# Performance work log

Measured on AMD Instinct MI355X. Metric: run time of the kernel, lower is better.

Reference implementation:

```python
import jax, jax.numpy as jnp
import numpy as np
import math

EPS = 1e-5  # torch BatchNorm2d default eps
EXPANSION_RATE = 2


def _bn_train(x, gamma, beta):
    # BatchNorm2d in training mode: biased batch statistics over (B, H, W)
    mu = jnp.mean(x, axis=(0, 2, 3), keepdims=True)
    var = jnp.var(x, axis=(0, 2, 3), keepdims=True)
    xn = (x - mu) * jax.lax.rsqrt(var + EPS)
    return gamma[None, :, None, None] * xn + beta[None, :, None, None]


def _conv1x1(x, w, b):
    # w: [O, C]  (1x1 conv kernel squeezed), b: [O]
    return jnp.einsum('bchw,oc->bohw', x, w) + b[None, :, None, None]


def _lsgc(x, w_diff, b_diff, g_bn, be_bn, w_in, b_in, g_ibn, be_ibn,
          w_mr, b_mr, g_mbn, be_mbn):
    B, C, H, W = x.shape
    bit_depth = max(math.ceil(math.log2(H)), math.ceil(math.log2(W)))
    steps = [EXPANSION_RATE * 2 ** (n - 1) for n in range(1, bit_depth + 1)]

    fmax = None
    for step in steps:
        for axis, size in ((3, W), (2, H)):
            s = step % size
            for sgn in (1, -1):  # forward / backward rolls
                shifted = jnp.roll(x, sgn * s, axis=axis) if s else x
                d = x - shifted
                fmax = d if fmax is None else jnp.maximum(fmax, d)

    x_diff = _bn_train(_conv1x1(fmax, w_diff, b_diff), g_bn, be_bn)
    x_proc = _bn_train(_conv1x1(x, w_in, b_in), g_ibn, be_ibn)

    # MRConv: concat -> 1x1 conv -> BN -> GELU (exact) -> residual add
    x_cat = jnp.concatenate([x_proc, x_diff], axis=1)
    h = _bn_train(_conv1x1(x_cat, w_mr, b_mr), g_mbn, be_mbn)
    h = jax.nn.gelu(h, approximate=False)
    return x_proc + h


def setup_inputs() -> dict:
    key = jax.random.key(0)
    ks = jax.random.split(key, 8)
    B, C_in, C_out, H, W = 32, 128, 128, 64, 64

    def kaiming(k, o, i):
        return jax.random.normal(k, (o, i), jnp.float32) * np.sqrt(2.0 / i)

    return {
        'x': jax.random.normal(ks[0], (B, C_in, H, W), jnp.float32),
        'w_diff': kaiming(ks[1], C_out, C_in),
        'b_diff': jnp.zeros((C_out,), jnp.float32),
        'g_bn': jnp.ones((C_out,), jnp.float32),
        'be_bn': jnp.zeros((C_out,), jnp.float32),
        'w_in': kaiming(ks[2], C_out, C_in),
        'b_in': jnp.zeros((C_out,), jnp.float32),
        'g_ibn': jnp.ones((C_out,), jnp.float32),
        'be_ibn': jnp.zeros((C_out,), jnp.float32),
        'w_mr': kaiming(ks[3], C_out, 2 * C_out),
        'b_mr': jnp.zeros((C_out,), jnp.float32),
        'g_mbn': jnp.ones((C_out,), jnp.float32),
        'be_mbn': jnp.zeros((C_out,), jnp.float32),
    }


def reference(x, w_diff, b_diff, g_bn, be_bn, w_in, b_in, g_ibn, be_ibn,
              w_mr, b_mr, g_mbn, be_mbn):
    return _lsgc(x, w_diff, b_diff, g_bn, be_bn, w_in, b_in, g_ibn, be_ibn,
                 w_mr, b_mr, g_mbn, be_mbn)
```

## Files before the change

### kernel.cpp

```cpp
#include <hip/hip_runtime.h>
#include <math.h>


#define INV_NPIX (1.0f / 131072.0f)
#define EPS 1e-5f
#define KP 66

typedef __attribute__((ext_vector_type(8))) short s16x8;
typedef __attribute__((ext_vector_type(4))) float f32x4;

__device__ __forceinline__ uint32_t bf16_rne(float v) {
  uint32_t x = __float_as_uint(v);
  return (x + 0x7fffu + ((x >> 16) & 1u)) >> 16;
}
__device__ __forceinline__ uint32_t pack_hl(float v) {
  uint32_t h = bf16_rne(v);
  float lo = v - __uint_as_float(h << 16);
  return h | (bf16_rne(lo) << 16);
}
__device__ __forceinline__ float bf_lo(uint32_t d) {
  return __uint_as_float(d << 16);
}
__device__ __forceinline__ float bf_hi(uint32_t d) {
  return __uint_as_float(d & 0xffff0000u);
}
__device__ __forceinline__ float4 fmin4(float4 a, float4 b) {
  return make_float4(fminf(a.x, b.x), fminf(a.y, b.y), fminf(a.z, b.z),
                     fminf(a.w, b.w));
}

__global__ __launch_bounds__(256) void stencil_prep_kernel(
    const float* __restrict__ x, uint32_t* __restrict__ xp,
    uint32_t* __restrict__ fp, const float* __restrict__ w_in,
    const float* __restrict__ w_diff, unsigned short* __restrict__ wInH,
    unsigned short* __restrict__ wInL, unsigned short* __restrict__ wDfH,
    unsigned short* __restrict__ wDfL) {
  __shared__ float4 pA[1024];
  __shared__ float4 pB[1024];
  if (blockIdx.x >= 2048) {
    const int t = (blockIdx.x - 2048) * 256 + threadIdx.x;
    const int e = t & 16383;
    const float* w = (t < 16384) ? w_in : w_diff;
    unsigned short* aH = (t < 16384) ? wInH : wDfH;
    unsigned short* aL = (t < 16384) ? wInL : wDfL;
    const int j = e & 7, l = (e >> 3) & 63, mt = (e >> 9) & 7, kc = e >> 12;
    const int m = mt * 16 + (l & 15);
    const int k = kc * 32 + ((l >> 4) << 3) + j;
    const uint32_t p = pack_hl(w[m * 128 + k]);
    aH[e] = (unsigned short)(p & 0xffffu);
    aL[e] = (unsigned short)(p >> 16);
    return;
  }
  const int b = blockIdx.x >> 6;
  const int cp = blockIdx.x & 63;
  const float4* xa = (const float4*)x + (size_t)(b * 128 + 2 * cp) * 1024;
  const float4* xb = xa + 1024;
  float4 sA[4], sB[4];
#pragma unroll
  for (int i = 0; i < 4; ++i) {
    const int u = threadIdx.x + i * 256;
    sA[i] = xa[u];
    sB[i] = xb[u];
    pA[u] = sA[i];
    pB[u] = sB[i];
  }
  __syncthreads();
  const size_t obase = (size_t)(b * 64 + cp) * 1024;
#pragma unroll
  for (int i = 0; i < 4; ++i) {
    const int u = threadIdx.x + i * 256;
    const int h = u >> 4, wu = u & 15;
    const int row = u & ~15;
    float4 mA, mB;
    {
      const float4 A = sA[i];
      const float4 L = pA[row | ((wu + 15) & 15)];
      const float4 R = pA[row | ((wu + 1) & 15)];
      float4 m = fmin4(A, fmin4(L, R));
      m = fmin4(m, make_float4(A.z, A.w, R.x, R.y));
      m = fmin4(m, make_float4(L.z, L.w, A.x, A.y));
      m = fmin4(m, pA[row | ((wu + 2) & 15)]);
      m = fmin4(m, pA[row | ((wu + 14) & 15)]);
      m = fmin4(m, pA[row | ((wu + 4) & 15)]);
      m = fmin4(m, pA[row | ((wu + 12) & 15)]);
      m = fmin4(m, pA[row | ((wu + 8) & 15)]);
      m = fmin4(m, pA[(((h + 2) & 63) << 4) | wu]);
      m = fmin4(m, pA[(((h + 62) & 63) << 4) | wu]);
      m = fmin4(m, pA[(((h + 4) & 63) << 4) | wu]);
      m = fmin4(m, pA[(((h + 60) & 63) << 4) | wu]);
      m = fmin4(m, pA[(((h + 8) & 63) << 4) | wu]);
      m = fmin4(m, pA[(((h + 56) & 63) << 4) | wu]);
      m = fmin4(m, pA[(((h + 16) & 63) << 4) | wu]);
      m = fmin4(m, pA[(((h + 48) & 63) << 4) | wu]);
      m = fmin4(m, pA[(((h + 32) & 63) << 4) | wu]);
      mA = m;
    }
    {
      const float4 A = sB[i];
      const float4 L = pB[row | ((wu + 15) & 15)];
      const float4 R = pB[row | ((wu + 1) & 15)];
      float4 m = fmin4(A, fmin4(L, R));
      m = fmin4(m, make_float4(A.z, A.w, R.x, R.y));
      m = fmin4(m, make_float4(L.z, L.w, A.x, A.y));
      m = fmin4(m, pB[row | ((wu + 2) & 15)]);
      m = fmin4(m, pB[row | ((wu + 14) & 15)]);
      m = fmin4(m, pB[row | ((wu + 4) & 15)]);
      m = fmin4(m, pB[row | ((wu + 12) & 15)]);
      m = fmin4(m, pB[row | ((wu + 8) & 15)]);
      m = fmin4(m, pB[(((h + 2) & 63) << 4) | wu]);
      m = fmin4(m, pB[(((h + 62) & 63) << 4) | wu]);
      m = fmin4(m, pB[(((h + 4) & 63) << 4) | wu]);
      m = fmin4(m, pB[(((h + 60) & 63) << 4) | wu]);
      m = fmin4(m, pB[(((h + 8) & 63) << 4) | wu]);
      m = fmin4(m, pB[(((h + 56) & 63) << 4) | wu]);
      m = fmin4(m, pB[(((h + 16) & 63) << 4) | wu]);
      m = fmin4(m, pB[(((h + 48) & 63) << 4) | wu]);
      m = fmin4(m, pB[(((h + 32) & 63) << 4) | wu]);
      mB = m;
    }
    uint4 px, pf;
    px.x = bf16_rne(sA[i].x) | (bf16_rne(sB[i].x) << 16);
    px.y = bf16_rne(sA[i].y) | (bf16_rne(sB[i].y) << 16);
    px.z = bf16_rne(sA[i].z) | (bf16_rne(sB[i].z) << 16);
    px.w = bf16_rne(sA[i].w) | (bf16_rne(sB[i].w) << 16);
    pf.x = bf16_rne(sA[i].x - mA.x) | (bf16_rne(sB[i].x - mB.x) << 16);
    pf.y = bf16_rne(sA[i].y - mA.y) | (bf16_rne(sB[i].y - mB.y) << 16);
    pf.z = bf16_rne(sA[i].z - mA.z) | (bf16_rne(sB[i].z - mB.z) << 16);
    pf.w = bf16_rne(sA[i].w - mA.w) | (bf16_rne(sB[i].w - mB.w) << 16);
    ((uint4*)xp)[obase + u] = px;
    ((uint4*)fp)[obase + u] = pf;
  }
}

template <int NC>
__device__ __forceinline__ void gemm_body(
    const unsigned short* __restrict__ AH, const unsigned short* __restrict__ AL,
    const uint32_t* __restrict__ B0, const uint32_t* __restrict__ B1,
    uint32_t* __restrict__ outp, float* __restrict__ pS,
    float* __restrict__ pQ, const int bx, uint32_t* Bs) {
  const int tid = threadIdx.x;
  const int lane = tid & 63;
  const int wave = tid >> 6;
  const int b = bx >> 6;
  const int hw0 = (bx & 63) << 6;
  const int sk2 = tid >> 4;
  const int sn4 = (tid & 15) << 2;
  const int q = lane >> 4;
  const int ln = lane & 15;

  f32x4 acc[2][4];
#pragma unroll
  for (int i = 0; i < 2; ++i)
#pragma unroll
    for (int j = 0; j < 4; ++j) acc[i][j] = (f32x4)(0.0f);

  uint4 ld[NC];
#pragma unroll
  for (int c = 0; c < NC; ++c) {
    const uint32_t* src = (c < 4) ? B0 : B1;
    ld[c] = *(const uint4*)&src[((size_t)(b * 64 + (c & 3) * 16 + sk2)) * 4096 +
                                hw0 + sn4];
  }
  s16x8 ah[2][2], al[2][2];
#pragma unroll
  for (int mt2 = 0; mt2 < 2; ++mt2) {
    const size_t off = ((size_t)((wave * 2 + mt2) * 64 + lane)) << 3;
    ah[0][mt2] = *(const s16x8*)(AH + off);
    al[0][mt2] = *(const s16x8*)(AL + off);
  }

#pragma unroll
  for (int kc = 0; kc < NC; ++kc) {
    const int cur = kc & 1;
    const int nxt = cur ^ 1;
    uint32_t* buf = Bs + cur * (16 * KP);
    *(uint4*)&buf[sk2 * KP + sn4] = ld[kc];
    __syncthreads();
    if (kc + 1 < NC) {
#pragma unroll
      for (int mt2 = 0; mt2 < 2; ++mt2) {
        const size_t off =
            ((size_t)(((kc + 1) * 8 + wave * 2 + mt2) * 64 + lane)) << 3;
        ah[nxt][mt2] = *(const s16x8*)(AH + off);
        al[nxt][mt2] = *(const s16x8*)(AL + off);
      }
    }
#pragma unroll
    for (int nt = 0; nt < 4; ++nt) {
      union { uint32_t u[4]; s16x8 s; } bb;
#pragma unroll
      for (int j = 0; j < 4; ++j)
        bb.u[j] = buf[(q * 4 + j) * KP + nt * 16 + ln];
#pragma unroll
      for (int mt2 = 0; mt2 < 2; ++mt2) {
        acc[mt2][nt] = __builtin_amdgcn_mfma_f32_16x16x32_bf16(
            ah[cur][mt2], bb.s, acc[mt2][nt], 0, 0, 0);
        acc[mt2][nt] = __builtin_amdgcn_mfma_f32_16x16x32_bf16(
            al[cur][mt2], bb.s, acc[mt2][nt], 0, 0, 0);
      }
    }
  }

#pragma unroll
  for (int mt2 = 0; mt2 < 2; ++mt2) {
    float sa[4] = {0.f, 0.f, 0.f, 0.f};
    float sq[4] = {0.f, 0.f, 0.f, 0.f};
#pragma unroll
    for (int nt = 0; nt < 4; ++nt) {
#pragma unroll
      for (int rp = 0; rp < 2; ++rp) {
        const float v0 = acc[mt2][nt][2 * rp];
        const float v1 = acc[mt2][nt][2 * rp + 1];
        const int m2 = (wave * 2 + mt2) * 8 + q * 2 + rp;
        outp[((size_t)(b * 64 + m2)) * 4096 + hw0 + nt * 16 + ln] =
            bf16_rne(v0) | (bf16_rne(v1) << 16);
        sa[2 * rp] += v0;
        sq[2 * rp] += v0 * v0;
        sa[2 * rp + 1] += v1;
        sq[2 * rp + 1] += v1 * v1;
      }
    }
#pragma unroll
    for (int off = 1; off < 16; off <<= 1) {
#pragma unroll
      for (int r = 0; r < 4; ++r) {
        sa[r] += __shfl_xor(sa[r], off);
        sq[r] += __shfl_xor(sq[r], off);
      }
    }
    if (ln == 0) {
#pragma unroll
      for (int r = 0; r < 4; ++r) {
        const int m = (wave * 2 + mt2) * 16 + q * 4 + r;
        pS[bx * 128 + m] = sa[r];
        pQ[bx * 128 + m] = sq[r];
      }
    }
  }
}

__global__ __launch_bounds__(256) void gemm1_dual(
    const unsigned short* __restrict__ AH1, const unsigned short* __restrict__ AL1,
    const uint32_t* __restrict__ XP, uint32_t* __restrict__ out1,
    float* __restrict__ sv1, float* __restrict__ sq1,
    const unsigned short* __restrict__ AH2, const unsigned short* __restrict__ AL2,
    const uint32_t* __restrict__ FP, uint32_t* __restrict__ out2,
    float* __restrict__ sv2, float* __restrict__ sq2) {
  __shared__ uint32_t Bs[2 * 16 * KP];
  const int bx = blockIdx.x & 2047;
  if ((blockIdx.x >> 11) == 0)
    gemm_body<4>(AH1, AL1, XP, nullptr, out1, sv1, sq1, bx, Bs);
  else
    gemm_body<4>(AH2, AL2, FP, nullptr, out2, sv2, sq2, bx, Bs);
}

__global__ __launch_bounds__(256) void gemm2_kernel(
    const unsigned short* __restrict__ AH, const unsigned short* __restrict__ AL,
    const uint32_t* __restrict__ B0, const uint32_t* __restrict__ B1,
    uint32_t* __restrict__ outp, float* __restrict__ sv,
    float* __restrict__ sq) {
  __shared__ uint32_t Bs[2 * 16 * KP];
  gemm_body<8>(AH, AL, B0, B1, outp, sv, sq, blockIdx.x, Bs);
}

__global__ __launch_bounds__(256) void reduce_kernel(
    const float* __restrict__ P, float* __restrict__ p2) {
  const int a = blockIdx.x >> 4, g = blockIdx.x & 15;
  const int c = threadIdx.x & 127, h = threadIdx.x >> 7;
  const float* src = P + ((size_t)(a * 2048 + g * 128 + h * 64)) * 128 + c;
  float s0 = 0.f, s1 = 0.f, s2 = 0.f, s3 = 0.f;
#pragma unroll
  for (int j = 0; j < 64; j += 4) {
    s0 += src[(j + 0) * 128];
    s1 += src[(j + 1) * 128];
    s2 += src[(j + 2) * 128];
    s3 += src[(j + 3) * 128];
  }
  __shared__ float sm[256];
  sm[threadIdx.x] = (s0 + s1) + (s2 + s3);
  __syncthreads();
  if (h == 0) p2[(a * 16 + g) * 128 + c] = sm[c] + sm[128 + c];
}

__global__ __launch_bounds__(256) void finalize1_kernel(
    const float* __restrict__ p2, const float* __restrict__ g_ibn,
    const float* __restrict__ be_ibn, const float* __restrict__ g_bn,
    const float* __restrict__ w_mr, float* __restrict__ a_in,
    float* __restrict__ d_in, unsigned short* __restrict__ wEffH,
    unsigned short* __restrict__ wEffL) {
  __shared__ float sa[256];
  const int t = threadIdx.x;
  if (t < 128) {
    float s = 0.f, qq = 0.f;
#pragma unroll
    for (int g = 0; g < 16; ++g) {
      s += p2[g * 128 + t];
      qq += p2[(16 + g) * 128 + t];
    }
    const float mu = s * INV_NPIX;
    const float var = fmaxf(qq * INV_NPIX - mu * mu, 0.f);
    const float a = g_ibn[t] * rsqrtf(var + EPS);
    if (blockIdx.x == 0) {
      a_in[t] = a;
      d_in[t] = be_ibn[t] - mu * a;
    }
    sa[t] = a;
  } else {
    const int c = t - 128;
    float s = 0.f, qq = 0.f;
#pragma unroll
    for (int g = 0; g < 16; ++g) {
      s += p2[(32 + g) * 128 + c];
      qq += p2[(48 + g) * 128 + c];
    }
    const float mu = s * INV_NPIX;
    const float var = fmaxf(qq * INV_NPIX - mu * mu, 0.f);
    sa[t] = g_bn[c] * rsqrtf(var + EPS);
  }
  __syncthreads();
  const int e = blockIdx.x * 256 + t;
  const int j = e & 7, l = (e >> 3) & 63, mt = (e >> 9) & 7, kc = e >> 12;
  const int m = mt * 16 + (l & 15);
  const int k = kc * 32 + ((l >> 4) << 3) + j;
  const uint32_t p = pack_hl(w_mr[m * 256 + k] * sa[k]);
  wEffH[e] = (unsigned short)(p & 0xffffu);
  wEffL[e] = (unsigned short)(p >> 16);
}

__global__ __launch_bounds__(128) void finalize2_kernel(
    const float* __restrict__ p2h, const float* __restrict__ g_mbn,
    const float* __restrict__ be_mbn, float* __restrict__ a_m,
    float* __restrict__ d_m) {
  const int t = threadIdx.x;
  float s = 0.f, qq = 0.f;
#pragma unroll
  for (int g = 0; g < 16; ++g) {
    s += p2h[g * 128 + t];
    qq += p2h[(16 + g) * 128 + t];
  }
  const float mu = s * INV_NPIX;
  const float var = fmaxf(qq * INV_NPIX - mu * mu, 0.f);
  const float a = g_mbn[t] * rsqrtf(var + EPS);
  a_m[t] = a;
  d_m[t] = be_mbn[t] - mu * a;
}

__device__ __forceinline__ float gelu_exact(float z) {
  return 0.5f * z * (1.0f + erff(z * 0.70710678118654752f));
}

__global__ __launch_bounds__(256) void epilogue_kernel(
    const uint32_t* __restrict__ yp, const uint32_t* __restrict__ hp,
    const float* __restrict__ a_in, const float* __restrict__ d_in,
    const float* __restrict__ a_m, const float* __restrict__ d_m,
    float* __restrict__ out) {
  const size_t i = (size_t)blockIdx.x * 256 + threadIdx.x;
  const int cp = (int)((i >> 10) & 63);
  const int b = (int)(i >> 16);
  const int c0 = 2 * cp, c1 = 2 * cp + 1;
  const uint4 yv = ((const uint4*)yp)[i];
  const uint4 hv = ((const uint4*)hp)[i];
  const float a0 = a_in[c0], d0 = d_in[c0], m0 = a_m[c0], e0 = d_m[c0];
  const float a1 = a_in[c1], d1 = d_in[c1], m1 = a_m[c1], e1 = d_m[c1];
  float4 o0, o1;
  o0.x = fmaf(a0, bf_lo(yv.x), d0) + gelu_exact(fmaf(m0, bf_lo(hv.x), e0));
  o0.y = fmaf(a0, bf_lo(yv.y), d0) + gelu_exact(fmaf(m0, bf_lo(hv.y), e0));
  o0.z = fmaf(a0, bf_lo(yv.z), d0) + gelu_exact(fmaf(m0, bf_lo(hv.z), e0));
  o0.w = fmaf(a0, bf_lo(yv.w), d0) + gelu_exact(fmaf(m0, bf_lo(hv.w), e0));
  o1.x = fmaf(a1, bf_hi(yv.x), d1) + gelu_exact(fmaf(m1, bf_hi(hv.x), e1));
  o1.y = fmaf(a1, bf_hi(yv.y), d1) + gelu_exact(fmaf(m1, bf_hi(hv.y), e1));
  o1.z = fmaf(a1, bf_hi(yv.z), d1) + gelu_exact(fmaf(m1, bf_hi(hv.z), e1));
  o1.w = fmaf(a1, bf_hi(yv.w), d1) + gelu_exact(fmaf(m1, bf_hi(hv.w), e1));
  const size_t u = i & 1023;
  ((float4*)out)[(size_t)(b * 128 + c0) * 1024 + u] = o0;
  ((float4*)out)[(size_t)(b * 128 + c1) * 1024 + u] = o1;
}

extern "C" void kernel_launch(void* const* d_in, const int* in_sizes, int n_in,
                              void* d_out, int out_size, void* d_ws,
                              size_t ws_size, hipStream_t stream) {
  const float* x = (const float*)d_in[0];
  const float* w_diff = (const float*)d_in[1];
  const float* g_bn = (const float*)d_in[3];
  const float* w_in = (const float*)d_in[5];
  const float* g_ibn = (const float*)d_in[7];
  const float* be_ibn = (const float*)d_in[8];
  const float* w_mr = (const float*)d_in[9];
  const float* g_mbn = (const float*)d_in[11];
  const float* be_mbn = (const float*)d_in[12];
  float* out = (float*)d_out;

  const size_t PD = (size_t)8388608;
  uint32_t* ws = (uint32_t*)d_ws;
  uint32_t* xp = ws;
  uint32_t* fpx = ws + PD;
  uint32_t* ypIn = ws + 2 * PD;
  uint32_t* ypDf = ws + 3 * PD;
  uint32_t* hp = ws + 4 * PD;
  float* st = (float*)(ws + 5 * PD);
  float* p2 = st;
  float* p2h = st + 8192;
  float* a_in = st + 12288, *dinc = st + 12416;
  float* a_m = st + 12544, *d_m = st + 12672;
  unsigned short* fr = (unsigned short*)(st + 12800);
  unsigned short* wInH = fr;
  unsigned short* wInL = fr + 16384;
  unsigned short* wDfH = fr + 32768;
  unsigned short* wDfL = fr + 49152;
  unsigned short* wEffH = fr + 65536;
  unsigned short* wEffL = fr + 98304;
  float* g1p = (float*)(ws + 4 * PD);
  float* g2p = (float*)ws;

  stencil_prep_kernel<<<2176, 256, 0, stream>>>(x, xp, fpx, w_in, w_diff,
                                                wInH, wInL, wDfH, wDfL);
  gemm1_dual<<<4096, 256, 0, stream>>>(wInH, wInL, xp, ypIn, g1p,
                                       g1p + 262144, wDfH, wDfL, fpx, ypDf,
                                       g1p + 524288, g1p + 786432);
  reduce_kernel<<<64, 256, 0, stream>>>(g1p, p2);
  finalize1_kernel<<<128, 256, 0, stream>>>(p2, g_ibn, be_ibn, g_bn, w_mr,
                                            a_in, dinc, wEffH, wEffL);
  gemm2_kernel<<<2048, 256, 0, stream>>>(wEffH, wEffL, ypIn, ypDf, hp, g2p,
                                         g2p + 262144);
  reduce_kernel<<<32, 256, 0, stream>>>(g2p, p2h);
  finalize2_kernel<<<1, 128, 0, stream>>>(p2h, g_mbn, be_mbn, a_m, d_m);
  epilogue_kernel<<<8192, 256, 0, stream>>>(ypIn, hp, a_in, dinc, a_m, d_m,
                                            out);
}
```

Baseline: 271.8 us.

## Make GEMM kernels process multiple tiles per block with cross-tile prefetch

Both GEMM stages now have each block loop over several consecutive 64-pixel tiles (4 for gemm1, 2 for gemm2), using fewer blocks. Each block loads a full 64-row K slab into LDS with a single barrier instead of one barrier per 16-row chunk. The next tile's (or next half's) B operand is prefetched into registers while the current tile is computed. This cuts launch and barrier overhead and hides global load latency, but LDS use per block rises and fewer blocks are launched, which may lower occupancy and latency hiding.

```diff
diff --git a/kernel.cpp b/kernel.cpp
--- a/kernel.cpp
+++ b/kernel.cpp
@@ -5,6 +5,8 @@
 #define INV_NPIX (1.0f / 131072.0f)
 #define EPS 1e-5f
 #define KP 66
+#define T1 4
+#define T2 2
 
 typedef __attribute__((ext_vector_type(8))) short s16x8;
 typedef __attribute__((ext_vector_type(4))) float f32x4;
@@ -132,75 +134,10 @@
   }
 }
 
-template <int NC>
-__device__ __forceinline__ void gemm_body(
-    const unsigned short* __restrict__ AH, const unsigned short* __restrict__ AL,
-    const uint32_t* __restrict__ B0, const uint32_t* __restrict__ B1,
-    uint32_t* __restrict__ outp, float* __restrict__ pS,
-    float* __restrict__ pQ, const int bx, uint32_t* Bs) {
-  const int tid = threadIdx.x;
-  const int lane = tid & 63;
-  const int wave = tid >> 6;
-  const int b = bx >> 6;
-  const int hw0 = (bx & 63) << 6;
-  const int sk2 = tid >> 4;
-  const int sn4 = (tid & 15) << 2;
-  const int q = lane >> 4;
-  const int ln = lane & 15;
-
-  f32x4 acc[2][4];
-#pragma unroll
-  for (int i = 0; i < 2; ++i)
-#pragma unroll
-    for (int j = 0; j < 4; ++j) acc[i][j] = (f32x4)(0.0f);
-
-  uint4 ld[NC];
-#pragma unroll
-  for (int c = 0; c < NC; ++c) {
-    const uint32_t* src = (c < 4) ? B0 : B1;
-    ld[c] = *(const uint4*)&src[((size_t)(b * 64 + (c & 3) * 16 + sk2)) * 4096 +
-                                hw0 + sn4];
-  }
-  s16x8 ah[2][2], al[2][2];
-#pragma unroll
-  for (int mt2 = 0; mt2 < 2; ++mt2) {
-    const size_t off = ((size_t)((wave * 2 + mt2) * 64 + lane)) << 3;
-    ah[0][mt2] = *(const s16x8*)(AH + off);
-    al[0][mt2] = *(const s16x8*)(AL + off);
-  }
-
-#pragma unroll
-  for (int kc = 0; kc < NC; ++kc) {
-    const int cur = kc & 1;
-    const int nxt = cur ^ 1;
-    uint32_t* buf = Bs + cur * (16 * KP);
-    *(uint4*)&buf[sk2 * KP + sn4] = ld[kc];
-    __syncthreads();
-    if (kc + 1 < NC) {
-#pragma unroll
-      for (int mt2 = 0; mt2 < 2; ++mt2) {
-        const size_t off =
-            ((size_t)(((kc + 1) * 8 + wave * 2 + mt2) * 64 + lane)) << 3;
-        ah[nxt][mt2] = *(const s16x8*)(AH + off);
-        al[nxt][mt2] = *(const s16x8*)(AL + off);
-      }
-    }
-#pragma unroll
-    for (int nt = 0; nt < 4; ++nt) {
-      union { uint32_t u[4]; s16x8 s; } bb;
-#pragma unroll
-      for (int j = 0; j < 4; ++j)
-        bb.u[j] = buf[(q * 4 + j) * KP + nt * 16 + ln];
-#pragma unroll
-      for (int mt2 = 0; mt2 < 2; ++mt2) {
-        acc[mt2][nt] = __builtin_amdgcn_mfma_f32_16x16x32_bf16(
-            ah[cur][mt2], bb.s, acc[mt2][nt], 0, 0, 0);
-        acc[mt2][nt] = __builtin_amdgcn_mfma_f32_16x16x32_bf16(
-            al[cur][mt2], bb.s, acc[mt2][nt], 0, 0, 0);
-      }
-    }
-  }
-
+__device__ __forceinline__ void cwrite_stats(
+    const f32x4 (&acc)[2][4], uint32_t* __restrict__ outp,
+    float* __restrict__ pS, float* __restrict__ pQ, const int bx, const int b,
+    const int hw0, const int wave, const int q, const int ln) {
 #pragma unroll
   for (int mt2 = 0; mt2 < 2; ++mt2) {
     float sa[4] = {0.f, 0.f, 0.f, 0.f};
@@ -239,6 +176,95 @@
   }
 }
 
+template <int T>
+__device__ __forceinline__ void gemm1_persist(
+    const unsigned short* __restrict__ AH, const unsigned short* __restrict__ AL,
+    const uint32_t* __restrict__ B0, uint32_t* __restrict__ outp,
+    float* __restrict__ pS, float* __restrict__ pQ, const int p,
+    uint32_t* Bs) {
+  const int tid = threadIdx.x;
+  const int lane = tid & 63;
+  const int wave = tid >> 6;
+  const int sk2 = tid >> 4;
+  const int sn4 = (tid & 15) << 2;
+  const int q = lane >> 4;
+  const int ln = lane & 15;
+
+  uint4 ld[4];
+  {
+    const int bx0 = p * T;
+    const int b = bx0 >> 6, hw0 = (bx0 & 63) << 6;
+#pragma unroll
+    for (int c = 0; c < 4; ++c)
+      ld[c] = *(const uint4*)&B0[((size_t)(b * 64 + c * 16 + sk2)) * 4096 +
+                                 hw0 + sn4];
+  }
+
+#pragma unroll
+  for (int t = 0; t < T; ++t) {
+    const int bx = p * T + t;
+    const int b = bx >> 6, hw0 = (bx & 63) << 6;
+    uint32_t* buf = Bs + (t & 1) * (64 * KP);
+
+#pragma unroll
+    for (int c = 0; c < 4; ++c)
+      *(uint4*)&buf[(c * 16 + sk2) * KP + sn4] = ld[c];
+
+    s16x8 ah[2][2], al[2][2];
+#pragma unroll
+    for (int mt2 = 0; mt2 < 2; ++mt2) {
+      const size_t off = ((size_t)((wave * 2 + mt2) * 64 + lane)) << 3;
+      ah[0][mt2] = *(const s16x8*)(AH + off);
+      al[0][mt2] = *(const s16x8*)(AL + off);
+    }
+    __syncthreads();
+
+    if (t + 1 < T) {
+      const int bn = bx + 1;
+      const int b2 = bn >> 6, hw2 = (bn & 63) << 6;
+#pragma unroll
+      for (int c = 0; c < 4; ++c)
+        ld[c] = *(const uint4*)&B0[((size_t)(b2 * 64 + c * 16 + sk2)) * 4096 +
+                                   hw2 + sn4];
+    }
+
+    f32x4 acc[2][4];
+#pragma unroll
+    for (int i = 0; i < 2; ++i)
+#pragma unroll
+      for (int j = 0; j < 4; ++j) acc[i][j] = (f32x4)(0.0f);
+
+#pragma unroll
+    for (int kc = 0; kc < 4; ++kc) {
+      if (kc < 3) {
+#pragma unroll
+        for (int mt2 = 0; mt2 < 2; ++mt2) {
+          const size_t off =
+              ((size_t)(((kc + 1) * 8 + wave * 2 + mt2) * 64 + lane)) << 3;
+          ah[(kc + 1) & 1][mt2] = *(const s16x8*)(AH + off);
+          al[(kc + 1) & 1][mt2] = *(const s16x8*)(AL + off);
+        }
+      }
+#pragma unroll
+      for (int nt = 0; nt < 4; ++nt) {
+        union { uint32_t u[4]; s16x8 s; } bb;
+#pragma unroll
+        for (int j = 0; j < 4; ++j)
+          bb.u[j] = buf[(kc * 16 + q * 4 + j) * KP + nt * 16 + ln];
+#pragma unroll
+        for (int mt2 = 0; mt2 < 2; ++mt2) {
+          acc[mt2][nt] = __builtin_amdgcn_mfma_f32_16x16x32_bf16(
+              ah[kc & 1][mt2], bb.s, acc[mt2][nt], 0, 0, 0);
+          acc[mt2][nt] = __builtin_amdgcn_mfma_f32_16x16x32_bf16(
+              al[kc & 1][mt2], bb.s, acc[mt2][nt], 0, 0, 0);
+        }
+      }
+    }
+
+    cwrite_stats(acc, outp, pS, pQ, bx, b, hw0, wave, q, ln);
+  }
+}
+
 __global__ __launch_bounds__(256) void gemm1_dual(
     const unsigned short* __restrict__ AH1, const unsigned short* __restrict__ AL1,
     const uint32_t* __restrict__ XP, uint32_t* __restrict__ out1,
@@ -246,12 +272,146 @@
     const unsigned short* __restrict__ AH2, const unsigned short* __restrict__ AL2,
     const uint32_t* __restrict__ FP, uint32_t* __restrict__ out2,
     float* __restrict__ sv2, float* __restrict__ sq2) {
-  __shared__ uint32_t Bs[2 * 16 * KP];
-  const int bx = blockIdx.x & 2047;
-  if ((blockIdx.x >> 11) == 0)
-    gemm_body<4>(AH1, AL1, XP, nullptr, out1, sv1, sq1, bx, Bs);
+  __shared__ uint32_t Bs[2 * 64 * KP];
+  const int p = blockIdx.x & 511;
+  if (blockIdx.x < 512)
+    gemm1_persist<T1>(AH1, AL1, XP, out1, sv1, sq1, p, Bs);
   else
-    gemm_body<4>(AH2, AL2, FP, nullptr, out2, sv2, sq2, bx, Bs);
+    gemm1_persist<T1>(AH2, AL2, FP, out2, sv2, sq2, p, Bs);
+}
+
+template <int T>
+__device__ __forceinline__ void gemm2_persist(
+    const unsigned short* __restrict__ AH, const unsigned short* __restrict__ AL,
+    const uint32_t* __restrict__ B0, const uint32_t* __restrict__ B1,
+    uint32_t* __restrict__ outp, float* __restrict__ pS,
+    float* __restrict__ pQ, const int p, uint32_t* Bs) {
+  const int tid = threadIdx.x;
+  const int lane = tid & 63;
+  const int wave = tid >> 6;
+  const int sk2 = tid >> 4;
+  const int sn4 = (tid & 15) << 2;
+  const int q = lane >> 4;
+  const int ln = lane & 15;
+
+  uint4 ld[4];
+  {
+    const int bx0 = p * T;
+    const int b = bx0 >> 6, hw0 = (bx0 & 63) << 6;
+#pragma unroll
+    for (int c = 0; c < 4; ++c)
+      ld[c] = *(const uint4*)&B0[((size_t)(b * 64 + c * 16 + sk2)) * 4096 +
+                                 hw0 + sn4];
+  }
+
+#pragma unroll
+  for (int t = 0; t < T; ++t) {
+    const int bx = p * T + t;
+    const int b = bx >> 6, hw0 = (bx & 63) << 6;
+
+    f32x4 acc[2][4];
+#pragma unroll
+    for (int i = 0; i < 2; ++i)
+#pragma unroll
+      for (int j = 0; j < 4; ++j) acc[i][j] = (f32x4)(0.0f);
+
+    s16x8 ah[2][2], al[2][2];
+
+    {
+      uint32_t* buf = Bs;
+#pragma unroll
+      for (int c = 0; c < 4; ++c)
+        *(uint4*)&buf[(c * 16 + sk2) * KP + sn4] = ld[c];
+#pragma unroll
+      for (int mt2 = 0; mt2 < 2; ++mt2) {
+        const size_t off = ((size_t)((wave * 2 + mt2) * 64 + lane)) << 3;
+        ah[0][mt2] = *(const s16x8*)(AH + off);
+        al[0][mt2] = *(const s16x8*)(AL + off);
+      }
+      __syncthreads();
+#pragma unroll
+      for (int c = 0; c < 4; ++c)
+        ld[c] = *(const uint4*)&B1[((size_t)(b * 64 + c * 16 + sk2)) * 4096 +
+                                   hw0 + sn4];
+#pragma unroll
+      for (int kc = 0; kc < 4; ++kc) {
+        if (kc < 3) {
+#pragma unroll
+          for (int mt2 = 0; mt2 < 2; ++mt2) {
+            const size_t off =
+                ((size_t)(((kc + 1) * 8 + wave * 2 + mt2) * 64 + lane)) << 3;
+            ah[(kc + 1) & 1][mt2] = *(const s16x8*)(AH + off);
+            al[(kc + 1) & 1][mt2] = *(const s16x8*)(AL + off);
+          }
+        }
+#pragma unroll
+        for (int nt = 0; nt < 4; ++nt) {
+          union { uint32_t u[4]; s16x8 s; } bb;
+#pragma unroll
+          for (int j = 0; j < 4; ++j)
+            bb.u[j] = buf[(kc * 16 + q * 4 + j) * KP + nt * 16 + ln];
+#pragma unroll
+          for (int mt2 = 0; mt2 < 2; ++mt2) {
+            acc[mt2][nt] = __builtin_amdgcn_mfma_f32_16x16x32_bf16(
+                ah[kc & 1][mt2], bb.s, acc[mt2][nt], 0, 0, 0);
+            acc[mt2][nt] = __builtin_amdgcn_mfma_f32_16x16x32_bf16(
+                al[kc & 1][mt2], bb.s, acc[mt2][nt], 0, 0, 0);
+          }
+        }
+      }
+    }
+
+    {
+      uint32_t* buf = Bs + 64 * KP;
+#pragma unroll
+      for (int c = 0; c < 4; ++c)
+        *(uint4*)&buf[(c * 16 + sk2) * KP + sn4] = ld[c];
+#pragma unroll
+      for (int mt2 = 0; mt2 < 2; ++mt2) {
+        const size_t off =
+            ((size_t)((4 * 8 + wave * 2 + mt2) * 64 + lane)) << 3;
+        ah[0][mt2] = *(const s16x8*)(AH + off);
+        al[0][mt2] = *(const s16x8*)(AL + off);
+      }
+      __syncthreads();
+      if (t + 1 < T) {
+        const int bn = bx + 1;
+        const int b2 = bn >> 6, hw2 = (bn & 63) << 6;
+#pragma unroll
+        for (int c = 0; c < 4; ++c)
+          ld[c] = *(const uint4*)&B0[((size_t)(b2 * 64 + c * 16 + sk2)) * 4096 +
+                                     hw2 + sn4];
+      }
+#pragma unroll
+      for (int kc = 4; kc < 8; ++kc) {
+        if (kc < 7) {
+#pragma unroll
+          for (int mt2 = 0; mt2 < 2; ++mt2) {
+            const size_t off =
+                ((size_t)(((kc + 1) * 8 + wave * 2 + mt2) * 64 + lane)) << 3;
+            ah[(kc + 1) & 1][mt2] = *(const s16x8*)(AH + off);
+            al[(kc + 1) & 1][mt2] = *(const s16x8*)(AL + off);
+          }
+        }
+#pragma unroll
+        for (int nt = 0; nt < 4; ++nt) {
+          union { uint32_t u[4]; s16x8 s; } bb;
+#pragma unroll
+          for (int j = 0; j < 4; ++j)
+            bb.u[j] = buf[((kc - 4) * 16 + q * 4 + j) * KP + nt * 16 + ln];
+#pragma unroll
+          for (int mt2 = 0; mt2 < 2; ++mt2) {
+            acc[mt2][nt] = __builtin_amdgcn_mfma_f32_16x16x32_bf16(
+                ah[kc & 1][mt2], bb.s, acc[mt2][nt], 0, 0, 0);
+            acc[mt2][nt] = __builtin_amdgcn_mfma_f32_16x16x32_bf16(
+                al[kc & 1][mt2], bb.s, acc[mt2][nt], 0, 0, 0);
+          }
+        }
+      }
+    }
+
+    cwrite_stats(acc, outp, pS, pQ, bx, b, hw0, wave, q, ln);
+  }
 }
 
 __global__ __launch_bounds__(256) void gemm2_kernel(
@@ -259,8 +419,8 @@
     const uint32_t* __restrict__ B0, const uint32_t* __restrict__ B1,
     uint32_t* __restrict__ outp, float* __restrict__ sv,
     float* __restrict__ sq) {
-  __shared__ uint32_t Bs[2 * 16 * KP];
-  gemm_body<8>(AH, AL, B0, B1, outp, sv, sq, blockIdx.x, Bs);
+  __shared__ uint32_t Bs[2 * 64 * KP];
+  gemm2_persist<T2>(AH, AL, B0, B1, outp, sv, sq, blockIdx.x, Bs);
 }
 
 __global__ __launch_bounds__(256) void reduce_kernel(
@@ -414,13 +574,13 @@
 
   stencil_prep_kernel<<<2176, 256, 0, stream>>>(x, xp, fpx, w_in, w_diff,
                                                 wInH, wInL, wDfH, wDfL);
-  gemm1_dual<<<4096, 256, 0, stream>>>(wInH, wInL, xp, ypIn, g1p,
+  gemm1_dual<<<1024, 256, 0, stream>>>(wInH, wInL, xp, ypIn, g1p,
                                        g1p + 262144, wDfH, wDfL, fpx, ypDf,
                                        g1p + 524288, g1p + 786432);
   reduce_kernel<<<64, 256, 0, stream>>>(g1p, p2);
   finalize1_kernel<<<128, 256, 0, stream>>>(p2, g_ibn, be_ibn, g_bn, w_mr,
                                             a_in, dinc, wEffH, wEffL);
-  gemm2_kernel<<<2048, 256, 0, stream>>>(wEffH, wEffL, ypIn, ypDf, hp, g2p,
+  gemm2_kernel<<<1024, 256, 0, stream>>>(wEffH, wEffL, ypIn, ypDf, hp, g2p,
                                          g2p + 262144);
   reduce_kernel<<<32, 256, 0, stream>>>(g2p, p2h);
   finalize2_kernel<<<1, 128, 0, stream>>>(p2h, g_mbn, be_mbn, a_m, d_m);
```

After: 253.4 us. -6.7%, faster.
